# Kernel optimization log

Measured on AMD Instinct MI355X. Metric: run time of the kernel, lower is better.

## Reference

```python
import jax, jax.numpy as jnp
import numpy as np

KERNEL = 3
PAD = (KERNEL - 1) // 2
KA = KERNEL * KERNEL          # kernel_area = 9
CENTER = KA // 2              # 4
CH_OUT = 64


def setup_inputs() -> dict:
    key = jax.random.key(0)
    k1, k2 = jax.random.split(key)
    x = jax.random.normal(k1, (8, 64, 128, 128), dtype=jnp.float32)
    weight = jax.random.uniform(k2, (1, 1, KA, 1, 1), dtype=jnp.float32)
    bias = jnp.zeros((1, 1, KA, 1, 1), dtype=jnp.float32)
    weight_center = jnp.ones((), dtype=jnp.float32)
    weight_median = jnp.ones((), dtype=jnp.float32)
    return {"x": x, "weight": weight, "bias": bias,
            "weight_center": weight_center, "weight_median": weight_median}


def _unfold_same(x):
    # x: (B, C, H, W) -> patches (B, C, KA, H, W), stride 1, zero pad
    B, C, H, W = x.shape
    xp = jnp.pad(x, ((0, 0), (0, 0), (PAD, PAD), (PAD, PAD)))
    # order matches F.unfold: index = ki*K + kj
    views = [xp[:, :, i:i + H, j:j + W] for i in range(KERNEL) for j in range(KERNEL)]
    return jnp.stack(views, axis=2)


def reference(x, weight, bias, weight_center, weight_median):
    B, C, H, W = x.shape
    x_sig = jax.nn.sigmoid(x)
    patches = _unfold_same(x_sig)                      # (B, C, KA, H, W)
    w = jax.nn.sigmoid(weight)
    b = jax.nn.sigmoid(bias)
    D = jnp.maximum(w, patches) + b                    # (B, C, KA, H, W)
    max_stat = jnp.sum(D, axis=2)
    # torch.median returns the lower middle element -> sort and index (KA-1)//2
    median_stat = jnp.sort(D, axis=2)[:, :, (KA - 1) // 2]
    mean_stat = jnp.mean(D, axis=2)
    center = patches[:, :, CENTER]
    out = (weight_center * center + weight_median * median_stat
           - max_stat - mean_stat)                     # (B, C, H, W)
    # expand to ch_out then sum over C_in -> every output channel is identical
    s = jnp.sum(out, axis=1)                           # (B, H, W)
    return jnp.broadcast_to(s[:, None], (B, CH_OUT, H, W))
```

## Files before the change

kernel.cpp:

```cpp
#include <hip/hip_runtime.h>

#define BATCH 8
#define CH    64
#define H     128
#define W     128
#define TW    32
#define TH    8
#define HWID  (TW + 2)
#define HHGT  (TH + 2)
#define HALO_N (HWID * HHGT)

__device__ __forceinline__ float sigmoidf_(float v) {
    return 1.0f / (1.0f + __expf(-v));
}

__global__ __launch_bounds__(256) void maxsig_kernel(
    const float* __restrict__ x,
    const float* __restrict__ weight,
    const float* __restrict__ bias,
    const float* __restrict__ wcp,
    const float* __restrict__ wmp,
    float* __restrict__ out)
{
    __shared__ float sm[HALO_N];

    const int tid = threadIdx.x;
    const int tx  = tid & (TW - 1);
    const int ty  = tid >> 5;
    const int bx  = blockIdx.x;
    const int by  = blockIdx.y;
    const int b   = blockIdx.z;

    const int i0 = tid;
    const int i1 = tid + 256;
    const bool has1 = (i1 < HALO_N);

    int yy0 = i0 / HWID, xx0 = i0 - yy0 * HWID;
    int sy0 = by * TH + yy0 - 1, sx0 = bx * TW + xx0 - 1;
    bool ok0 = (sy0 >= 0 && sy0 < H && sx0 >= 0 && sx0 < W);
    int off0 = min(max(sy0, 0), H - 1) * W + min(max(sx0, 0), W - 1);

    int i1c = has1 ? i1 : (HALO_N - 1);
    int yy1 = i1c / HWID, xx1 = i1c - yy1 * HWID;
    int sy1 = by * TH + yy1 - 1, sx1 = bx * TW + xx1 - 1;
    bool ok1 = (sy1 >= 0 && sy1 < H && sx1 >= 0 && sx1 < W);
    int off1 = min(max(sy1, 0), H - 1) * W + min(max(sx1, 0), W - 1);

    float wk[9], bk[9];
    #pragma unroll
    for (int k = 0; k < 9; ++k) {
        wk[k] = sigmoidf_(weight[k]);
        bk[k] = sigmoidf_(bias[k]);
    }
    const float wc = wcp[0];
    const float wm = wmp[0];

    const float* xb = x + (size_t)b * CH * H * W;

    float r0 = xb[off0];
    float r1 = xb[off1];

    float acc = 0.0f;

    for (int c = 0; c < CH; ++c) {
        sm[i0] = ok0 ? sigmoidf_(r0) : 0.0f;
        if (has1) sm[i1] = ok1 ? sigmoidf_(r1) : 0.0f;
        __syncthreads();

        if (c + 1 < CH) {
            const float* xn = xb + (size_t)(c + 1) * H * W;
            r0 = xn[off0];
            r1 = xn[off1];
        }

        float p[9];
        #pragma unroll
        for (int dy = 0; dy < 3; ++dy)
            #pragma unroll
            for (int dx = 0; dx < 3; ++dx)
                p[dy * 3 + dx] = sm[(ty + dy) * HWID + (tx + dx)];

        float d[9];
        float sum = 0.0f;
        #pragma unroll
        for (int k = 0; k < 9; ++k) {
            d[k] = fmaxf(wk[k], p[k]) + bk[k];
            sum += d[k];
        }

        #define S2(a,bb) { float t = d[a]; d[a] = fminf(d[a], d[bb]); d[bb] = fmaxf(t, d[bb]); }
        S2(0,3) S2(1,4) S2(2,5) S2(0,1) S2(0,2) S2(4,5) S2(3,5)
        S2(1,2) S2(3,4) S2(1,3) S2(1,6) S2(4,6) S2(2,6)
        S2(2,3) S2(4,7) S2(2,4) S2(3,7)
        S2(4,8) S2(3,8) S2(3,4)
        #undef S2
        const float med = d[4];

        acc += wc * p[4] + wm * med - sum - sum * (1.0f / 9.0f);

        __syncthreads();
    }

    float* op = out + (size_t)b * CH * H * W + (size_t)(by * TH + ty) * W + bx * TW + tx;
    #pragma unroll
    for (int co = 0; co < CH; ++co)
        op[(size_t)co * H * W] = acc;
}

extern "C" void kernel_launch(void* const* d_in, const int* in_sizes, int n_in,
                              void* d_out, int out_size, void* d_ws, size_t ws_size,
                              hipStream_t stream) {
    const float* x      = (const float*)d_in[0];
    const float* weight = (const float*)d_in[1];
    const float* bias   = (const float*)d_in[2];
    const float* wcp    = (const float*)d_in[3];
    const float* wmp    = (const float*)d_in[4];
    float* out = (float*)d_out;

    dim3 grid(W / TW, H / TH, BATCH);
    maxsig_kernel<<<grid, 256, 0, stream>>>(x, weight, bias, wcp, wmp, out);
}
```

Measured before the change: 116.8 us.

## Split channel reduction across blocks, full-row tiles, two rows per thread

Splits the 64-channel reduction into 8 chunks that run as separate blocks, which raises the block count from 512 to 2048. Each block now covers full-width rows, and each thread computes two vertically adjacent output pixels so the overlapping halo rows it reads are reused. Partial sums go into the output buffer, and a second kernel adds the 8 partials and broadcasts the result to all 64 output channels. The aim is more parallelism and fewer redundant shared-memory loads, at the cost of a second launch and an extra read-modify-write pass over the output.

```diff
diff --git a/kernel.cpp b/kernel.cpp
--- a/kernel.cpp
+++ b/kernel.cpp
@@ -1,20 +1,22 @@
 #include <hip/hip_runtime.h>
 
-#define BATCH 8
-#define CH    64
-#define H     128
-#define W     128
-#define TW    32
-#define TH    8
-#define HWID  (TW + 2)
-#define HHGT  (TH + 2)
+#define BATCH  8
+#define CH     64
+#define H      128
+#define W      128
+#define TH     4
+#define CHUNK  8
+#define NCHUNK (CH / CHUNK)
+#define HWID   (W + 2)
+#define HHGT   (TH + 2)
 #define HALO_N (HWID * HHGT)
+#define NSLOT  4
 
 __device__ __forceinline__ float sigmoidf_(float v) {
     return 1.0f / (1.0f + __expf(-v));
 }
 
-__global__ __launch_bounds__(256) void maxsig_kernel(
+__global__ __launch_bounds__(256) void partial_kernel(
     const float* __restrict__ x,
     const float* __restrict__ weight,
     const float* __restrict__ bias,
@@ -24,27 +26,27 @@
 {
     __shared__ float sm[HALO_N];
 
-    const int tid = threadIdx.x;
-    const int tx  = tid & (TW - 1);
-    const int ty  = tid >> 5;
-    const int bx  = blockIdx.x;
-    const int by  = blockIdx.y;
-    const int b   = blockIdx.z;
+    const int tid  = threadIdx.x;
+    const int tx   = tid & (W - 1);
+    const int ty0  = (tid >> 7) * 2;
+    const int by   = blockIdx.x;
+    const int chnk = blockIdx.y;
+    const int b    = blockIdx.z;
 
-    const int i0 = tid;
-    const int i1 = tid + 256;
-    const bool has1 = (i1 < HALO_N);
-
-    int yy0 = i0 / HWID, xx0 = i0 - yy0 * HWID;
-    int sy0 = by * TH + yy0 - 1, sx0 = bx * TW + xx0 - 1;
-    bool ok0 = (sy0 >= 0 && sy0 < H && sx0 >= 0 && sx0 < W);
-    int off0 = min(max(sy0, 0), H - 1) * W + min(max(sx0, 0), W - 1);
-
-    int i1c = has1 ? i1 : (HALO_N - 1);
-    int yy1 = i1c / HWID, xx1 = i1c - yy1 * HWID;
-    int sy1 = by * TH + yy1 - 1, sx1 = bx * TW + xx1 - 1;
-    bool ok1 = (sy1 >= 0 && sy1 < H && sx1 >= 0 && sx1 < W);
-    int off1 = min(max(sy1, 0), H - 1) * W + min(max(sx1, 0), W - 1);
+    bool has[NSLOT], ok[NSLOT];
+    int  off[NSLOT];
+    #pragma unroll
+    for (int s = 0; s < NSLOT; ++s) {
+        int i  = tid + s * 256;
+        has[s] = (i < HALO_N);
+        int ic = has[s] ? i : (HALO_N - 1);
+        int yy = ic / HWID;
+        int xx = ic - yy * HWID;
+        int sy = by * TH + yy - 1;
+        int sx = xx - 1;
+        ok[s]  = (sy >= 0 && sy < H && sx >= 0 && sx < W);
+        off[s] = min(max(sy, 0), H - 1) * W + min(max(sx, 0), W - 1);
+    }
 
     float wk[9], bk[9];
     #pragma unroll
@@ -55,56 +57,84 @@
     const float wc = wcp[0];
     const float wm = wmp[0];
 
-    const float* xb = x + (size_t)b * CH * H * W;
+    const float* xb = x + ((size_t)b * CH + chnk * CHUNK) * H * W;
 
-    float r0 = xb[off0];
-    float r1 = xb[off1];
+    float r[NSLOT];
+    #pragma unroll
+    for (int s = 0; s < NSLOT; ++s) r[s] = xb[off[s]];
 
-    float acc = 0.0f;
+    float acc0 = 0.0f, acc1 = 0.0f;
 
-    for (int c = 0; c < CH; ++c) {
-        sm[i0] = ok0 ? sigmoidf_(r0) : 0.0f;
-        if (has1) sm[i1] = ok1 ? sigmoidf_(r1) : 0.0f;
+    for (int c = 0; c < CHUNK; ++c) {
+        #pragma unroll
+        for (int s = 0; s < NSLOT; ++s)
+            if (has[s]) sm[tid + s * 256] = ok[s] ? sigmoidf_(r[s]) : 0.0f;
         __syncthreads();
 
-        if (c + 1 < CH) {
+        if (c + 1 < CHUNK) {
             const float* xn = xb + (size_t)(c + 1) * H * W;
-            r0 = xn[off0];
-            r1 = xn[off1];
+            #pragma unroll
+            for (int s = 0; s < NSLOT; ++s) r[s] = xn[off[s]];
         }
 
-        float p[9];
+        float v[4][3];
         #pragma unroll
-        for (int dy = 0; dy < 3; ++dy)
+        for (int dy = 0; dy < 4; ++dy)
             #pragma unroll
             for (int dx = 0; dx < 3; ++dx)
-                p[dy * 3 + dx] = sm[(ty + dy) * HWID + (tx + dx)];
+                v[dy][dx] = sm[(ty0 + dy) * HWID + tx + dx];
 
-        float d[9];
-        float sum = 0.0f;
         #pragma unroll
-        for (int k = 0; k < 9; ++k) {
-            d[k] = fmaxf(wk[k], p[k]) + bk[k];
-            sum += d[k];
+        for (int j = 0; j < 2; ++j) {
+            float d[9];
+            float sum = 0.0f;
+            #pragma unroll
+            for (int dy = 0; dy < 3; ++dy)
+                #pragma unroll
+                for (int dx = 0; dx < 3; ++dx) {
+                    int k = dy * 3 + dx;
+                    float dk = fmaxf(wk[k], v[j + dy][dx]) + bk[k];
+                    d[k] = dk;
+                    sum += dk;
+                }
+            const float center = v[j + 1][1];
+
+            #define S2(a,bb) { float t = d[a]; d[a] = fminf(d[a], d[bb]); d[bb] = fmaxf(t, d[bb]); }
+            S2(0,3) S2(1,4) S2(2,5) S2(0,1) S2(0,2) S2(4,5) S2(3,5)
+            S2(1,2) S2(3,4) S2(1,3) S2(1,6) S2(4,6) S2(2,6)
+            S2(2,3) S2(4,7) S2(2,4) S2(3,7)
+            S2(4,8) S2(3,8) S2(3,4)
+            #undef S2
+            const float med = d[4];
+
+            const float r_ = wc * center + wm * med - sum - sum * (1.0f / 9.0f);
+            if (j == 0) acc0 += r_; else acc1 += r_;
         }
-
-        #define S2(a,bb) { float t = d[a]; d[a] = fminf(d[a], d[bb]); d[bb] = fmaxf(t, d[bb]); }
-        S2(0,3) S2(1,4) S2(2,5) S2(0,1) S2(0,2) S2(4,5) S2(3,5)
-        S2(1,2) S2(3,4) S2(1,3) S2(1,6) S2(4,6) S2(2,6)
-        S2(2,3) S2(4,7) S2(2,4) S2(3,7)
-        S2(4,8) S2(3,8) S2(3,4)
-        #undef S2
-        const float med = d[4];
-
-        acc += wc * p[4] + wm * med - sum - sum * (1.0f / 9.0f);
 
         __syncthreads();
     }
 
-    float* op = out + (size_t)b * CH * H * W + (size_t)(by * TH + ty) * W + bx * TW + tx;
+    float* op = out + ((size_t)b * CH + chnk) * H * W
+                    + (size_t)(by * TH + ty0) * W + tx;
+    op[0] = acc0;
+    op[W] = acc1;
+}
+
+__global__ __launch_bounds__(256) void broadcast_kernel(float* __restrict__ out)
+{
+    const int g = blockIdx.x * 256 + threadIdx.x;
+    const int b = g >> 14;
+    const int p = g & 16383;
+    float* base = out + (size_t)b * CH * H * W;
+
+    float s = 0.0f;
+    #pragma unroll
+    for (int k = 0; k < NCHUNK; ++k)
+        s += base[(size_t)k * H * W + p];
+
     #pragma unroll
     for (int co = 0; co < CH; ++co)
-        op[(size_t)co * H * W] = acc;
+        base[(size_t)co * H * W + p] = s;
 }
 
 extern "C" void kernel_launch(void* const* d_in, const int* in_sizes, int n_in,
@@ -117,6 +147,9 @@
     const float* wmp    = (const float*)d_in[4];
     float* out = (float*)d_out;
 
-    dim3 grid(W / TW, H / TH, BATCH);
-    maxsig_kernel<<<grid, 256, 0, stream>>>(x, weight, bias, wcp, wmp, out);
+    dim3 grid1(H / TH, NCHUNK, BATCH);
+    partial_kernel<<<grid1, 256, 0, stream>>>(x, weight, bias, wcp, wmp, out);
+
+    const int npix = BATCH * H * W;
+    broadcast_kernel<<<npix / 256, 256, 0, stream>>>(out);
 }
```

Result: faster. 113.7 us (-2.7%).

## Split into channel-parallel partial sums with atomics plus vectorized broadcast kernel

Applied to the files above, without the earlier changes.

Replaces the single kernel, where each block looped over all 64 channels through shared memory, with a three-stage pipeline. A memset clears a workspace, then a partial kernel splits channels across blocks and accumulates into it with atomics. Each wavefront covers a full 128-wide row strip, two columns per lane, takes horizontal neighbours through lane shuffles and slides a register window down the rows, so no shared memory or barriers are needed. A separate broadcast kernel writes the 64 identical output channels with vectorized nontemporal stores. The gains in parallelism and write bandwidth cost two extra launches, atomic traffic and recomputing sigmoid on the three rows each strip reloads.

```diff
diff --git a/kernel.cpp b/kernel.cpp
--- a/kernel.cpp
+++ b/kernel.cpp
@@ -1,50 +1,66 @@
 #include <hip/hip_runtime.h>
 
-#define BATCH 8
-#define CH    64
-#define H     128
-#define W     128
-#define TW    32
-#define TH    8
-#define HWID  (TW + 2)
-#define HHGT  (TH + 2)
-#define HALO_N (HWID * HHGT)
+#define BATCH  8
+#define CH     64
+#define H      128
+#define W      128
+#define HW     (H * W)
+#define RS     8
+#define CPW    2
+#define NSTRIP (H / RS)
+
+typedef float vfloat2 __attribute__((ext_vector_type(2)));
+typedef float vfloat4 __attribute__((ext_vector_type(4)));
 
 __device__ __forceinline__ float sigmoidf_(float v) {
     return 1.0f / (1.0f + __expf(-v));
 }
 
-__global__ __launch_bounds__(256) void maxsig_kernel(
+__device__ __forceinline__ float pixel_val(
+    const float p0, const float p1, const float p2,
+    const float p3, const float p4, const float p5,
+    const float p6, const float p7, const float p8,
+    const float* __restrict__ wk, const float* __restrict__ bk,
+    const float wc, const float wm)
+{
+    float d[9];
+    d[0] = fmaxf(wk[0], p0) + bk[0];
+    d[1] = fmaxf(wk[1], p1) + bk[1];
+    d[2] = fmaxf(wk[2], p2) + bk[2];
+    d[3] = fmaxf(wk[3], p3) + bk[3];
+    d[4] = fmaxf(wk[4], p4) + bk[4];
+    d[5] = fmaxf(wk[5], p5) + bk[5];
+    d[6] = fmaxf(wk[6], p6) + bk[6];
+    d[7] = fmaxf(wk[7], p7) + bk[7];
+    d[8] = fmaxf(wk[8], p8) + bk[8];
+    float sum = ((d[0] + d[1]) + (d[2] + d[3])) + ((d[5] + d[6]) + (d[7] + d[8])) + d[4];
+
+    #define S2(a,bb) { float t = d[a]; d[a] = fminf(d[a], d[bb]); d[bb] = fmaxf(t, d[bb]); }
+    S2(0,3) S2(1,4) S2(2,5) S2(0,1) S2(0,2) S2(4,5) S2(3,5)
+    S2(1,2) S2(3,4) S2(1,3) S2(1,6) S2(4,6) S2(2,6)
+    S2(2,3) S2(4,7) S2(2,4) S2(3,7)
+    S2(4,8) S2(3,8) S2(3,4)
+    #undef S2
+
+    return wc * p4 + wm * d[4] - sum - sum * (1.0f / 9.0f);
+}
+
+__global__ __launch_bounds__(256) void partial_kernel(
     const float* __restrict__ x,
     const float* __restrict__ weight,
     const float* __restrict__ bias,
     const float* __restrict__ wcp,
     const float* __restrict__ wmp,
-    float* __restrict__ out)
+    float* __restrict__ s)
 {
-    __shared__ float sm[HALO_N];
+    const int tid   = threadIdx.x;
+    const int lane  = tid & 63;
+    const int strip = blockIdx.x * 4 + (tid >> 6);
+    const int c0    = blockIdx.y * CPW;
+    const int b     = blockIdx.z;
 
-    const int tid = threadIdx.x;
-    const int tx  = tid & (TW - 1);
-    const int ty  = tid >> 5;
-    const int bx  = blockIdx.x;
-    const int by  = blockIdx.y;
-    const int b   = blockIdx.z;
-
-    const int i0 = tid;
-    const int i1 = tid + 256;
-    const bool has1 = (i1 < HALO_N);
-
-    int yy0 = i0 / HWID, xx0 = i0 - yy0 * HWID;
-    int sy0 = by * TH + yy0 - 1, sx0 = bx * TW + xx0 - 1;
-    bool ok0 = (sy0 >= 0 && sy0 < H && sx0 >= 0 && sx0 < W);
-    int off0 = min(max(sy0, 0), H - 1) * W + min(max(sx0, 0), W - 1);
-
-    int i1c = has1 ? i1 : (HALO_N - 1);
-    int yy1 = i1c / HWID, xx1 = i1c - yy1 * HWID;
-    int sy1 = by * TH + yy1 - 1, sx1 = bx * TW + xx1 - 1;
-    bool ok1 = (sy1 >= 0 && sy1 < H && sx1 >= 0 && sx1 < W);
-    int off1 = min(max(sy1, 0), H - 1) * W + min(max(sx1, 0), W - 1);
+    const int row0 = strip * RS;
+    const int col  = 2 * lane;
 
     float wk[9], bk[9];
     #pragma unroll
@@ -55,56 +71,73 @@
     const float wc = wcp[0];
     const float wm = wmp[0];
 
-    const float* xb = x + (size_t)b * CH * H * W;
+    vfloat2 acc[RS];
+    #pragma unroll
+    for (int j = 0; j < RS; ++j) acc[j] = (vfloat2)(0.0f);
 
-    float r0 = xb[off0];
-    float r1 = xb[off1];
+    #pragma unroll
+    for (int cc = 0; cc < CPW; ++cc) {
+        const float* base = x + ((size_t)b * CH + c0 + cc) * HW + col;
 
-    float acc = 0.0f;
+        float L0, A0, B0, R0, L1, A1, B1, R1, L2, A2, B2, R2;
 
-    for (int c = 0; c < CH; ++c) {
-        sm[i0] = ok0 ? sigmoidf_(r0) : 0.0f;
-        if (has1) sm[i1] = ok1 ? sigmoidf_(r1) : 0.0f;
-        __syncthreads();
-
-        if (c + 1 < CH) {
-            const float* xn = xb + (size_t)(c + 1) * H * W;
-            r0 = xn[off0];
-            r1 = xn[off1];
+        #define LOADROW(ri, Lr, Ar, Br, Rr)                                   \
+        {                                                                     \
+            const int  r_   = (ri);                                           \
+            const bool okr  = (r_ >= 0) & (r_ < H);                           \
+            const int  rcl  = min(max(r_, 0), H - 1);                         \
+            vfloat2 v = *(const vfloat2*)(base + rcl * W);                    \
+            Ar = okr ? sigmoidf_(v.x) : 0.0f;                                 \
+            Br = okr ? sigmoidf_(v.y) : 0.0f;                                 \
+            float lf = __shfl_up(Br, 1);                                      \
+            float rg = __shfl_down(Ar, 1);                                    \
+            Lr = (lane == 0)  ? 0.0f : lf;                                    \
+            Rr = (lane == 63) ? 0.0f : rg;                                    \
         }
 
-        float p[9];
+        LOADROW(row0 - 1, L0, A0, B0, R0);
+        LOADROW(row0,     L1, A1, B1, R1);
+
         #pragma unroll
-        for (int dy = 0; dy < 3; ++dy)
-            #pragma unroll
-            for (int dx = 0; dx < 3; ++dx)
-                p[dy * 3 + dx] = sm[(ty + dy) * HWID + (tx + dx)];
+        for (int j = 0; j < RS; ++j) {
+            LOADROW(row0 + j + 1, L2, A2, B2, R2);
 
-        float d[9];
-        float sum = 0.0f;
-        #pragma unroll
-        for (int k = 0; k < 9; ++k) {
-            d[k] = fmaxf(wk[k], p[k]) + bk[k];
-            sum += d[k];
+            acc[j].x += pixel_val(L0, A0, B0,
+                                  L1, A1, B1,
+                                  L2, A2, B2, wk, bk, wc, wm);
+            acc[j].y += pixel_val(A0, B0, R0,
+                                  A1, B1, R1,
+                                  A2, B2, R2, wk, bk, wc, wm);
+
+            L0 = L1; A0 = A1; B0 = B1; R0 = R1;
+            L1 = L2; A1 = A2; B1 = B2; R1 = R2;
         }
-
-        #define S2(a,bb) { float t = d[a]; d[a] = fminf(d[a], d[bb]); d[bb] = fmaxf(t, d[bb]); }
-        S2(0,3) S2(1,4) S2(2,5) S2(0,1) S2(0,2) S2(4,5) S2(3,5)
-        S2(1,2) S2(3,4) S2(1,3) S2(1,6) S2(4,6) S2(2,6)
-        S2(2,3) S2(4,7) S2(2,4) S2(3,7)
-        S2(4,8) S2(3,8) S2(3,4)
-        #undef S2
-        const float med = d[4];
-
-        acc += wc * p[4] + wm * med - sum - sum * (1.0f / 9.0f);
-
-        __syncthreads();
+        #undef LOADROW
     }
 
-    float* op = out + (size_t)b * CH * H * W + (size_t)(by * TH + ty) * W + bx * TW + tx;
+    float* sp = s + (size_t)b * HW + col;
     #pragma unroll
-    for (int co = 0; co < CH; ++co)
-        op[(size_t)co * H * W] = acc;
+    for (int j = 0; j < RS; ++j) {
+        atomicAdd(sp + (size_t)(row0 + j) * W,     acc[j].x);
+        atomicAdd(sp + (size_t)(row0 + j) * W + 1, acc[j].y);
+    }
+}
+
+__global__ __launch_bounds__(256) void broadcast_kernel(
+    const float* __restrict__ s,
+    float* __restrict__ out)
+{
+    const int g  = (blockIdx.x * 256 + threadIdx.x) * 4;
+    const int b  = g >> 14;
+    const int p  = g & (HW - 1);
+    const int c0 = blockIdx.y * 16;
+
+    vfloat4 v = *(const vfloat4*)(s + (size_t)b * HW + p);
+
+    float* base = out + ((size_t)b * CH + c0) * HW + p;
+    #pragma unroll
+    for (int j = 0; j < 16; ++j)
+        __builtin_nontemporal_store(v, (vfloat4*)(base + (size_t)j * HW));
 }
 
 extern "C" void kernel_launch(void* const* d_in, const int* in_sizes, int n_in,
@@ -116,7 +149,13 @@
     const float* wcp    = (const float*)d_in[3];
     const float* wmp    = (const float*)d_in[4];
     float* out = (float*)d_out;
+    float* s   = (float*)d_ws;
 
-    dim3 grid(W / TW, H / TH, BATCH);
-    maxsig_kernel<<<grid, 256, 0, stream>>>(x, weight, bias, wcp, wmp, out);
+    hipMemsetAsync(s, 0, (size_t)BATCH * HW * sizeof(float), stream);
+
+    dim3 grid1(NSTRIP / 4, CH / CPW, BATCH);
+    partial_kernel<<<grid1, 256, 0, stream>>>(x, weight, bias, wcp, wmp, s);
+
+    dim3 grid2(BATCH * HW / (4 * 256), CH / 16);
+    broadcast_kernel<<<grid2, 256, 0, stream>>>(s, out);
 }
```

Result: slower. 137.2 us (+17.4%).

## Split into sigmoid-pad pass and channel-split stencil reduction with broadcast

Applied to the files above, without the earlier changes.

The single fused kernel is replaced by two. The first applies sigmoid to x and writes it into a zero-padded workspace. The second computes the 3x3 statistics straight from global memory, splits the 64 channels across four thread groups, reduces through shared memory, and writes the broadcast output with nontemporal stores. It also hoists the bias-sum algebra and adds a fast path for when all bias values are equal (true for the test input, where bias is zero), and it makes the parameters wave-uniform with readfirstlane. The aim is more parallelism per output pixel and fewer barriers, at the cost of an extra full write and read of a padded intermediate.

```diff
diff --git a/kernel.cpp b/kernel.cpp
--- a/kernel.cpp
+++ b/kernel.cpp
@@ -1,110 +1,147 @@
 #include <hip/hip_runtime.h>
 
-#define BATCH 8
-#define CH    64
-#define H     128
-#define W     128
-#define TW    32
-#define TH    8
-#define HWID  (TW + 2)
-#define HHGT  (TH + 2)
-#define HALO_N (HWID * HHGT)
+#define BATCH   8
+#define CH      64
+#define H       128
+#define W       128
+#define HW      (H * W)
+#define SPW     132
+#define SPH     130
+#define SPPLANE (SPH * SPW)
 
 __device__ __forceinline__ float sigmoidf_(float v) {
     return 1.0f / (1.0f + __expf(-v));
 }
 
-__global__ __launch_bounds__(256) void maxsig_kernel(
-    const float* __restrict__ x,
+__device__ __forceinline__ float uni_(float v) {
+    return __int_as_float(__builtin_amdgcn_readfirstlane(__float_as_int(v)));
+}
+
+__device__ __forceinline__ float med9_(float d[9]) {
+    #define S2(a,bb) { float t_ = d[a]; d[a] = fminf(d[a], d[bb]); d[bb] = fmaxf(t_, d[bb]); }
+    S2(0,3) S2(1,4) S2(2,5) S2(0,1) S2(0,2) S2(4,5) S2(3,5)
+    S2(1,2) S2(3,4) S2(1,3) S2(1,6) S2(4,6) S2(2,6)
+    S2(2,3) S2(4,7) S2(2,4) S2(3,7)
+    S2(4,8) S2(3,8) S2(3,4)
+    #undef S2
+    return d[4];
+}
+
+__global__ __launch_bounds__(256) void sig_pad_kernel(
+    const float* __restrict__ x, float* __restrict__ sp)
+{
+    const int t  = blockIdx.x * 256 + threadIdx.x;
+    const int j  = t & 63;
+    const int r  = (t >> 6) & 127;
+    const int bc = t >> 13;
+
+    const float* xp  = x  + (size_t)bc * HW + (size_t)r * W;
+    float*       pl  = sp + (size_t)bc * SPPLANE;
+    float*       row = pl + (size_t)(r + 1) * SPW;
+
+    row[j + 1]  = sigmoidf_(xp[j]);
+    row[j + 65] = sigmoidf_(xp[j + 64]);
+
+    if (j == 0)  row[0]   = 0.0f;
+    if (j == 63) row[129] = 0.0f;
+    if (r == 0) {
+        pl[j] = 0.0f; pl[j + 64] = 0.0f;
+        if (j == 0) { pl[128] = 0.0f; pl[129] = 0.0f; }
+    }
+    if (r == 127) {
+        float* bp = pl + (size_t)129 * SPW;
+        bp[j] = 0.0f; bp[j + 64] = 0.0f;
+        if (j == 0) { bp[128] = 0.0f; bp[129] = 0.0f; }
+    }
+}
+
+template <bool UNIF>
+__device__ __forceinline__ float px_term(
+    const float* __restrict__ q,
+    const float* __restrict__ wk, const float* __restrict__ bk,
+    float wc, float wm, float SB, float b0)
+{
+    const float p0 = q[0],           p1 = q[1],           p2 = q[2];
+    const float p3 = q[SPW],         p4 = q[SPW + 1],     p5 = q[SPW + 2];
+    const float p6 = q[2 * SPW],     p7 = q[2 * SPW + 1], p8 = q[2 * SPW + 2];
+
+    float m[9];
+    m[0] = fmaxf(wk[0], p0); m[1] = fmaxf(wk[1], p1); m[2] = fmaxf(wk[2], p2);
+    m[3] = fmaxf(wk[3], p3); m[4] = fmaxf(wk[4], p4); m[5] = fmaxf(wk[5], p5);
+    m[6] = fmaxf(wk[6], p6); m[7] = fmaxf(wk[7], p7); m[8] = fmaxf(wk[8], p8);
+    const float sum_m = ((m[0] + m[1]) + (m[2] + m[3]))
+                      + ((m[5] + m[6]) + (m[7] + m[8])) + m[4];
+
+    float med;
+    if (UNIF) {
+        med = med9_(m) + b0;
+    } else {
+        float d[9];
+        #pragma unroll
+        for (int k = 0; k < 9; ++k) d[k] = m[k] + bk[k];
+        med = med9_(d);
+    }
+
+    const float sumD = sum_m + SB;
+    return wc * p4 + wm * med - sumD - sumD * (1.0f / 9.0f);
+}
+
+__global__ __launch_bounds__(256) void reduce_bcast_kernel(
+    const float* __restrict__ sp,
     const float* __restrict__ weight,
     const float* __restrict__ bias,
     const float* __restrict__ wcp,
     const float* __restrict__ wmp,
     float* __restrict__ out)
 {
-    __shared__ float sm[HALO_N];
+    __shared__ float red[4][64];
 
     const int tid = threadIdx.x;
-    const int tx  = tid & (TW - 1);
-    const int ty  = tid >> 5;
-    const int bx  = blockIdx.x;
-    const int by  = blockIdx.y;
-    const int b   = blockIdx.z;
-
-    const int i0 = tid;
-    const int i1 = tid + 256;
-    const bool has1 = (i1 < HALO_N);
-
-    int yy0 = i0 / HWID, xx0 = i0 - yy0 * HWID;
-    int sy0 = by * TH + yy0 - 1, sx0 = bx * TW + xx0 - 1;
-    bool ok0 = (sy0 >= 0 && sy0 < H && sx0 >= 0 && sx0 < W);
-    int off0 = min(max(sy0, 0), H - 1) * W + min(max(sx0, 0), W - 1);
-
-    int i1c = has1 ? i1 : (HALO_N - 1);
-    int yy1 = i1c / HWID, xx1 = i1c - yy1 * HWID;
-    int sy1 = by * TH + yy1 - 1, sx1 = bx * TW + xx1 - 1;
-    bool ok1 = (sy1 >= 0 && sy1 < H && sx1 >= 0 && sx1 < W);
-    int off1 = min(max(sy1, 0), H - 1) * W + min(max(sx1, 0), W - 1);
+    const int px  = tid & 63;
+    const int g   = tid >> 6;
+    const int blk = blockIdx.x;
+    const int hh  = blk & 1;
+    const int r   = (blk >> 1) & 127;
+    const int b   = blk >> 8;
+    const int j   = hh * 64 + px;
 
     float wk[9], bk[9];
     #pragma unroll
     for (int k = 0; k < 9; ++k) {
-        wk[k] = sigmoidf_(weight[k]);
-        bk[k] = sigmoidf_(bias[k]);
+        wk[k] = uni_(sigmoidf_(weight[k]));
+        bk[k] = uni_(sigmoidf_(bias[k]));
     }
-    const float wc = wcp[0];
-    const float wm = wmp[0];
+    const float wc = uni_(wcp[0]);
+    const float wm = uni_(wmp[0]);
+    const float SB = ((bk[0] + bk[1]) + (bk[2] + bk[3]))
+                   + ((bk[5] + bk[6]) + (bk[7] + bk[8])) + bk[4];
+    const float b0 = bk[0];
+    const bool unif = (bk[0] == bk[1]) & (bk[1] == bk[2]) & (bk[2] == bk[3])
+                    & (bk[3] == bk[4]) & (bk[4] == bk[5]) & (bk[5] == bk[6])
+                    & (bk[6] == bk[7]) & (bk[7] == bk[8]);
 
-    const float* xb = x + (size_t)b * CH * H * W;
-
-    float r0 = xb[off0];
-    float r1 = xb[off1];
+    const float* base = sp + ((size_t)b * CH + g * 16) * SPPLANE
+                           + (size_t)r * SPW + j;
 
     float acc = 0.0f;
-
-    for (int c = 0; c < CH; ++c) {
-        sm[i0] = ok0 ? sigmoidf_(r0) : 0.0f;
-        if (has1) sm[i1] = ok1 ? sigmoidf_(r1) : 0.0f;
-        __syncthreads();
-
-        if (c + 1 < CH) {
-            const float* xn = xb + (size_t)(c + 1) * H * W;
-            r0 = xn[off0];
-            r1 = xn[off1];
-        }
-
-        float p[9];
-        #pragma unroll
-        for (int dy = 0; dy < 3; ++dy)
-            #pragma unroll
-            for (int dx = 0; dx < 3; ++dx)
-                p[dy * 3 + dx] = sm[(ty + dy) * HWID + (tx + dx)];
-
-        float d[9];
-        float sum = 0.0f;
-        #pragma unroll
-        for (int k = 0; k < 9; ++k) {
-            d[k] = fmaxf(wk[k], p[k]) + bk[k];
-            sum += d[k];
-        }
-
-        #define S2(a,bb) { float t = d[a]; d[a] = fminf(d[a], d[bb]); d[bb] = fmaxf(t, d[bb]); }
-        S2(0,3) S2(1,4) S2(2,5) S2(0,1) S2(0,2) S2(4,5) S2(3,5)
-        S2(1,2) S2(3,4) S2(1,3) S2(1,6) S2(4,6) S2(2,6)
-        S2(2,3) S2(4,7) S2(2,4) S2(3,7)
-        S2(4,8) S2(3,8) S2(3,4)
-        #undef S2
-        const float med = d[4];
-
-        acc += wc * p[4] + wm * med - sum - sum * (1.0f / 9.0f);
-
-        __syncthreads();
+    if (unif) {
+        #pragma unroll 2
+        for (int c = 0; c < 16; ++c)
+            acc += px_term<true >(base + (size_t)c * SPPLANE, wk, bk, wc, wm, SB, b0);
+    } else {
+        #pragma unroll 2
+        for (int c = 0; c < 16; ++c)
+            acc += px_term<false>(base + (size_t)c * SPPLANE, wk, bk, wc, wm, SB, b0);
     }
 
-    float* op = out + (size_t)b * CH * H * W + (size_t)(by * TH + ty) * W + bx * TW + tx;
+    red[g][px] = acc;
+    __syncthreads();
+    const float s = (red[0][px] + red[1][px]) + (red[2][px] + red[3][px]);
+
+    float* op = out + ((size_t)b * CH + g * 16) * HW + (size_t)r * W + j;
     #pragma unroll
-    for (int co = 0; co < CH; ++co)
-        op[(size_t)co * H * W] = acc;
+    for (int co = 0; co < 16; ++co)
+        __builtin_nontemporal_store(s, op + (size_t)co * HW);
 }
 
 extern "C" void kernel_launch(void* const* d_in, const int* in_sizes, int n_in,
@@ -116,7 +153,11 @@
     const float* wcp    = (const float*)d_in[3];
     const float* wmp    = (const float*)d_in[4];
     float* out = (float*)d_out;
+    float* sp  = (float*)d_ws;
 
-    dim3 grid(W / TW, H / TH, BATCH);
-    maxsig_kernel<<<grid, 256, 0, stream>>>(x, weight, bias, wcp, wmp, out);
+    const int n0 = BATCH * CH * H * 64;
+    sig_pad_kernel<<<n0 / 256, 256, 0, stream>>>(x, sp);
+
+    const int n1 = BATCH * H * 2;
+    reduce_bcast_kernel<<<n1, 256, 0, stream>>>(sp, weight, bias, wcp, wmp, out);
 }
```

Result: no change. 117.5 us (+0.6%).
